# Kernel optimization log

Measured on AMD Instinct MI355X. Metric: run time of the kernel, lower is better.

The kernel has to match this reference:

```python
import jax, jax.numpy as jnp
import numpy as np

DIM = 768
NUM_HEADS = 12
HEAD_DIM = DIM // NUM_HEADS
SCALE = HEAD_DIM ** -0.5


def setup_inputs() -> dict:
    key = jax.random.key(0)
    k_x, k_qw, k_qb, k_pw, k_pb = jax.random.split(key, 5)
    B, S = 4, 2048
    x = jax.random.normal(k_x, (B, S, DIM), dtype=jnp.float32)
    # torch nn.Linear convention: weight shape [out_features, in_features]
    qkv_w = jax.random.normal(k_qw, (2 * DIM, DIM), dtype=jnp.float32) * 0.02
    qkv_b = jax.random.normal(k_qb, (2 * DIM,), dtype=jnp.float32) * 0.02
    proj_w = jax.random.normal(k_pw, (DIM, DIM), dtype=jnp.float32) * 0.02
    proj_b = jax.random.normal(k_pb, (DIM,), dtype=jnp.float32) * 0.02
    return {"x": x, "qkv_w": qkv_w, "qkv_b": qkv_b, "proj_w": proj_w, "proj_b": proj_b}


def reference(x, qkv_w, qkv_b, proj_w, proj_b):
    B, S, D = x.shape
    H, Hd = NUM_HEADS, HEAD_DIM
    # qkv projection -> (B, S, 2*D)
    qkv = jnp.einsum('bsd,ed->bse', x, qkv_w) + qkv_b
    # reshape to (B, S, 2, H, Hd) then split q, v with heads leading: (B, H, S, Hd)
    qkv = qkv.reshape(B, S, 2, H, Hd).transpose(2, 0, 3, 1, 4)
    q, v = qkv[0], qkv[1]
    q = q * SCALE
    # shared Q=K scores: (B, H, S, S)
    attn = jnp.einsum('bhid,bhjd->bhij', q, q)
    attn = jax.nn.softmax(attn, axis=-1)  # attn_drop p=0 (identity)
    out = jnp.einsum('bhij,bhjd->bhid', attn, v)
    out = out.transpose(0, 2, 1, 3).reshape(B, S, D)
    out = jnp.einsum('bsd,ed->bse', out, proj_w) + proj_b  # proj_drop p=0
    return out
```

## Files before the change

kernel.cpp:

```cpp
#include <hip/hip_runtime.h>
#include <hip/hip_bf16.h>

#define NH 12
#define HD 64
#define SEQ 2048
#define DM 768

typedef __attribute__((ext_vector_type(8))) short bf16x8;
typedef __attribute__((ext_vector_type(4))) short bf16x4;
typedef __attribute__((ext_vector_type(4))) float f32x4;

static __device__ __forceinline__ unsigned short f2bf(float f) {
  unsigned int u = __float_as_uint(f);
  u += 0x7fff + ((u >> 16) & 1);
  return (unsigned short)(u >> 16);
}

static __device__ __forceinline__ unsigned cvt_pk_bf16(float lo, float hi) {
  unsigned r;
  asm("v_cvt_pk_bf16_f32 %0, %1, %2" : "=v"(r) : "v"(lo), "v"(hi));
  return r;
}

static __device__ __forceinline__ void gload_lds16(const void* g, void* l) {
  __builtin_amdgcn_global_load_lds(
      (const __attribute__((address_space(1))) void*)g,
      (__attribute__((address_space(3))) void*)l, 16, 0, 0);
}

static __device__ __forceinline__ bf16x8 cat4(bf16x4 a, bf16x4 b) {
  bf16x8 r;
  r[0] = a[0]; r[1] = a[1]; r[2] = a[2]; r[3] = a[3];
  r[4] = b[0]; r[5] = b[1]; r[6] = b[2]; r[7] = b[3];
  return r;
}

#define QSCALE 0.15014030f

__global__ __launch_bounds__(256) void cvt3_kernel(
    const float* __restrict__ s0, unsigned short* __restrict__ d0, int n0,
    const float* __restrict__ s1, unsigned short* __restrict__ d1, int n1,
    const float* __restrict__ s2, unsigned short* __restrict__ d2, int n2) {
  int i = blockIdx.x * 256 + threadIdx.x;
  const int stride = gridDim.x * 256;
  const int ntot = n0 + n1 + n2;
  for (; i < ntot; i += stride) {
    const float* src;
    unsigned short* dst;
    int j = i;
    if (j < n0) { src = s0; dst = d0; }
    else if (j < n0 + n1) { j -= n0; src = s1; dst = d1; }
    else { j -= n0 + n1; src = s2; dst = d2; }
    const float4 a = reinterpret_cast<const float4*>(src)[j * 2];
    const float4 b = reinterpret_cast<const float4*>(src)[j * 2 + 1];
    ushort4 lo = make_ushort4(f2bf(a.x), f2bf(a.y), f2bf(a.z), f2bf(a.w));
    ushort4 hi = make_ushort4(f2bf(b.x), f2bf(b.y), f2bf(b.z), f2bf(b.w));
    reinterpret_cast<ushort4*>(dst)[j * 2] = lo;
    reinterpret_cast<ushort4*>(dst)[j * 2 + 1] = hi;
  }
}

__global__ __launch_bounds__(256) void qkv_kernel(
    const unsigned short* __restrict__ xb, const unsigned short* __restrict__ wb,
    const float* __restrict__ bias,
    unsigned short* __restrict__ qb, unsigned short* __restrict__ vtb) {
  __shared__ alignas(16) char As[2][8192];
  __shared__ alignas(16) char Bs[2][8192];
  const int tid = threadIdx.x;
  const int lane = tid & 63, wid = tid >> 6;
  const int wr = wid >> 1, wc = wid & 1;
  const int g = lane >> 4, c = lane & 15;
  const int m0 = blockIdx.x * 128, n0 = blockIdx.y * 128;
  const char* Ab = (const char*)xb;
  const char* Bb = (const char*)wb;

  const int o0 = tid * 16, o1 = tid * 16 + 4096;
  const int r0 = o0 >> 6, r1 = o1 >> 6;
  const int sw0 = (o0 & 63) ^ (((r0 >> 1) & 3) << 4);
  const int sw1 = (o1 & 63) ^ (((r1 >> 1) & 3) << 4);

  auto stage = [&](int kt, int buf) {
    const int k0b = kt * 64;
    gload_lds16(Ab + (size_t)(m0 + r0) * 1536 + k0b + sw0, &As[buf][o0]);
    gload_lds16(Bb + (size_t)(n0 + r0) * 1536 + k0b + sw0, &Bs[buf][o0]);
    gload_lds16(Ab + (size_t)(m0 + r1) * 1536 + k0b + sw1, &As[buf][o1]);
    gload_lds16(Bb + (size_t)(n0 + r1) * 1536 + k0b + sw1, &Bs[buf][o1]);
  };

  f32x4 acc[4][4] = {};
  stage(0, 0);

  for (int kt = 0; kt < 24; ++kt) {
    __syncthreads();
    if (kt < 23) stage(kt + 1, (kt + 1) & 1);
    const char* Ap = As[kt & 1];
    const char* Bp = Bs[kt & 1];
    bf16x8 a_f[4], b_f[4];
#pragma unroll
    for (int i = 0; i < 4; ++i) {
      const int ra = wr * 64 + i * 16 + c;
      const int rb = wc * 64 + i * 16 + c;
      a_f[i] = *reinterpret_cast<const bf16x8*>(Ap + ra * 64 + ((g ^ ((ra >> 1) & 3)) << 4));
      b_f[i] = *reinterpret_cast<const bf16x8*>(Bp + rb * 64 + ((g ^ ((rb >> 1) & 3)) << 4));
    }
#pragma unroll
    for (int ai = 0; ai < 4; ++ai)
#pragma unroll
      for (int ni = 0; ni < 4; ++ni)
        acc[ai][ni] = __builtin_amdgcn_mfma_f32_16x16x32_bf16(a_f[ai], b_f[ni], acc[ai][ni], 0, 0, 0);
  }

#pragma unroll
  for (int ni = 0; ni < 4; ++ni) {
    const int n = n0 + wc * 64 + ni * 16 + c;
    const float bn = bias[n];
    if (n < DM) {
      const int h = n >> 6, d = n & 63;
#pragma unroll
      for (int ai = 0; ai < 4; ++ai)
#pragma unroll
        for (int r = 0; r < 4; ++r) {
          const int m = m0 + wr * 64 + ai * 16 + g * 4 + r;
          const int bb = m >> 11, s = m & 2047;
          qb[(((size_t)(bb * NH + h)) * SEQ + s) * HD + d] = f2bf((acc[ai][ni][r] + bn) * QSCALE);
        }
    } else {
      const int nn = n - DM;
      const int h = nn >> 6, d = nn & 63;
#pragma unroll
      for (int ai = 0; ai < 4; ++ai) {
        const int m_base = m0 + wr * 64 + ai * 16 + g * 4;
        const int bb = m_base >> 11, s0 = m_base & 2047;
        const int blk = s0 >> 5, off = s0 & 31;
        const int offp = (((off >> 4) & 1) << 2) + (((off >> 2) & 3) << 3);
        ushort4 pk = make_ushort4(f2bf(acc[ai][ni][0] + bn), f2bf(acc[ai][ni][1] + bn),
                                  f2bf(acc[ai][ni][2] + bn), f2bf(acc[ai][ni][3] + bn));
        *reinterpret_cast<ushort4*>(
            &vtb[((size_t)(bb * NH + h) * HD + d) * SEQ + blk * 32 + offp]) = pk;
      }
    }
  }
}

__global__ __launch_bounds__(256, 4) void attn_kernel(
    const unsigned short* __restrict__ qb, const unsigned short* __restrict__ vtb,
    unsigned short* __restrict__ ao) {
  __shared__ alignas(16) char pool[2][16384];

  const int tid = threadIdx.x;
  const int lane = tid & 63, wid = tid >> 6;
  const int g = lane >> 4, c = lane & 15;
  const int wq = wid >> 1, wk = wid & 1;

  const int wg = blockIdx.x;
  const int xcd = wg & 7;
  const int idx = wg >> 3;
  const int bh = xcd * 6 + (idx >> 5);
  const int qs0 = (idx & 31) * 64;
  const size_t base = (size_t)bh * SEQ * HD;

  bf16x8 qf[2][2];
#pragma unroll
  for (int jq = 0; jq < 2; ++jq) {
    const unsigned short* qrow = &qb[base + (size_t)(qs0 + wq * 32 + jq * 16 + c) * HD + g * 8];
    qf[jq][0] = *reinterpret_cast<const bf16x8*>(qrow);
    qf[jq][1] = *reinterpret_cast<const bf16x8*>(qrow + 32);
  }

  const char* qbB = (const char*)qb;
  const char* vtB = (const char*)vtb;
  const int oK0 = tid * 16, oK1 = tid * 16 + 4096;
  const int swK0 = oK0 ^ (((oK0 >> 7) & 7) << 4);
  const int swK1 = oK1 ^ (((oK1 >> 7) & 7) << 4);
  const int rV0 = oK0 >> 7, rV1 = oK1 >> 7;
  const int swV0 = (oK0 & 127) ^ ((rV0 & 7) << 4);
  const int swV1 = (oK1 & 127) ^ ((rV1 & 7) << 4);

  auto stage = [&](int t, int buf) {
    char* P = pool[buf];
    const size_t kQ = base * 2 + (size_t)t * 8192;
    gload_lds16(qbB + kQ + swK0, P + oK0);
    gload_lds16(qbB + kQ + swK1, P + oK1);
    gload_lds16(vtB + ((size_t)(bh * HD + rV0) * SEQ + t * 64) * 2 + swV0, P + 8192 + oK0);
    gload_lds16(vtB + ((size_t)(bh * HD + rV1) * SEQ + t * 64) * 2 + swV1, P + 8192 + oK1);
  };

  float l_p[2] = {0.f, 0.f};
  f32x4 o_acc[4][2] = {};

  const int cswz = (c & 7) << 4;

  stage(0, 0);
  asm volatile("s_waitcnt vmcnt(0)" ::: "memory");
  __builtin_amdgcn_sched_barrier(0);
  __builtin_amdgcn_s_barrier();

  for (int t = 0; t < 32; ++t) {
    const char* P = pool[t & 1];
    if (t < 31) stage(t + 1, (t + 1) & 1);

    f32x4 sa[2][2] = {};
    __builtin_amdgcn_s_setprio(1);
#pragma unroll
    for (int jp = 0; jp < 2; ++jp) {
      const int krow = wk * 32 + jp * 16 + c;
      const bf16x8 kf0 = *reinterpret_cast<const bf16x8*>(P + krow * 128 + ((g * 16) ^ cswz));
      const bf16x8 kf1 = *reinterpret_cast<const bf16x8*>(P + krow * 128 + ((64 + g * 16) ^ cswz));
#pragma unroll
      for (int jq = 0; jq < 2; ++jq) {
        sa[jp][jq] = __builtin_amdgcn_mfma_f32_16x16x32_bf16(kf0, qf[jq][0], sa[jp][jq], 0, 0, 0);
        sa[jp][jq] = __builtin_amdgcn_mfma_f32_16x16x32_bf16(kf1, qf[jq][1], sa[jp][jq], 0, 0, 0);
      }
    }
    __builtin_amdgcn_s_setprio(0);

    bf16x4 pb[2][2];
#pragma unroll
    for (int jp = 0; jp < 2; ++jp)
#pragma unroll
      for (int jq = 0; jq < 2; ++jq) {
        float p0 = __builtin_amdgcn_exp2f(sa[jp][jq][0]);
        float p1 = __builtin_amdgcn_exp2f(sa[jp][jq][1]);
        float p2 = __builtin_amdgcn_exp2f(sa[jp][jq][2]);
        float p3 = __builtin_amdgcn_exp2f(sa[jp][jq][3]);
        l_p[jq] += (p0 + p1) + (p2 + p3);
        uint2 wv = make_uint2(cvt_pk_bf16(p0, p1), cvt_pk_bf16(p2, p3));
        pb[jp][jq] = *reinterpret_cast<bf16x4*>(&wv);
      }

    bf16x8 pvv[2];
    pvv[0] = cat4(pb[0][0], pb[1][0]);
    pvv[1] = cat4(pb[0][1], pb[1][1]);
    __builtin_amdgcn_s_setprio(1);
#pragma unroll
    for (int dn = 0; dn < 4; ++dn) {
      const int vrow = dn * 16 + c;
      const bf16x8 av = *reinterpret_cast<const bf16x8*>(
          P + 8192 + vrow * 128 + ((wk * 64 + 16 * g) ^ ((vrow & 7) << 4)));
#pragma unroll
      for (int jq = 0; jq < 2; ++jq)
        o_acc[dn][jq] = __builtin_amdgcn_mfma_f32_16x16x32_bf16(av, pvv[jq], o_acc[dn][jq], 0, 0, 0);
    }
    __builtin_amdgcn_s_setprio(0);

    asm volatile("s_waitcnt vmcnt(0)" ::: "memory");
    __builtin_amdgcn_sched_barrier(0);
    __builtin_amdgcn_s_barrier();
  }

#pragma unroll
  for (int jq = 0; jq < 2; ++jq) {
    float v = l_p[jq];
    v += __shfl_xor(v, 16);
    v += __shfl_xor(v, 32);
    l_p[jq] = v;
  }

  float* ex = (float*)(pool[0] + wq * 16384);
  float* exl = ex + 32 * 68;
  if (wk == 1) {
#pragma unroll
    for (int dn = 0; dn < 4; ++dn)
#pragma unroll
      for (int jq = 0; jq < 2; ++jq)
        *reinterpret_cast<f32x4*>(&ex[(jq * 16 + c) * 68 + dn * 16 + 4 * g]) = o_acc[dn][jq];
    if (g == 0) {
      exl[c] = l_p[0];
      exl[16 + c] = l_p[1];
    }
  }
  __syncthreads();
  if (wk == 0) {
    const int b = bh / NH, h = bh % NH;
    float linv[2];
#pragma unroll
    for (int jq = 0; jq < 2; ++jq)
      linv[jq] = __builtin_amdgcn_rcpf(l_p[jq] + exl[jq * 16 + c]);
#pragma unroll
    for (int dn = 0; dn < 4; ++dn)
#pragma unroll
      for (int jq = 0; jq < 2; ++jq) {
        f32x4 o = o_acc[dn][jq];
        o += *reinterpret_cast<const f32x4*>(&ex[(jq * 16 + c) * 68 + dn * 16 + 4 * g]);
        uint2 wv = make_uint2(cvt_pk_bf16(o[0] * linv[jq], o[1] * linv[jq]),
                              cvt_pk_bf16(o[2] * linv[jq], o[3] * linv[jq]));
        *reinterpret_cast<uint2*>(
            &ao[((size_t)b * SEQ + qs0 + wq * 32 + jq * 16 + c) * DM + h * HD + dn * 16 + 4 * g]) = wv;
      }
  }
}

__global__ __launch_bounds__(256) void proj_kernel(
    const unsigned short* __restrict__ ao, const unsigned short* __restrict__ pwb,
    const float* __restrict__ bias, float* __restrict__ out) {
  __shared__ alignas(16) char As[2][8192];
  __shared__ alignas(16) char Bs[2][8192];
  const int tid = threadIdx.x;
  const int lane = tid & 63, wid = tid >> 6;
  const int wr = wid >> 1, wc = wid & 1;
  const int g = lane >> 4, c = lane & 15;
  const int m0 = blockIdx.x * 128, n0 = blockIdx.y * 128;
  const char* Ab = (const char*)ao;
  const char* Bb = (const char*)pwb;

  const int o0 = tid * 16, o1 = tid * 16 + 4096;
  const int r0 = o0 >> 6, r1 = o1 >> 6;
  const int sw0 = (o0 & 63) ^ (((r0 >> 1) & 3) << 4);
  const int sw1 = (o1 & 63) ^ (((r1 >> 1) & 3) << 4);

  auto stage = [&](int kt, int buf) {
    const int k0b = kt * 64;
    gload_lds16(Ab + (size_t)(m0 + r0) * 1536 + k0b + sw0, &As[buf][o0]);
    gload_lds16(Bb + (size_t)(n0 + r0) * 1536 + k0b + sw0, &Bs[buf][o0]);
    gload_lds16(Ab + (size_t)(m0 + r1) * 1536 + k0b + sw1, &As[buf][o1]);
    gload_lds16(Bb + (size_t)(n0 + r1) * 1536 + k0b + sw1, &Bs[buf][o1]);
  };

  f32x4 acc[4][4] = {};
  stage(0, 0);

  for (int kt = 0; kt < 24; ++kt) {
    __syncthreads();
    if (kt < 23) stage(kt + 1, (kt + 1) & 1);
    const char* Ap = As[kt & 1];
    const char* Bp = Bs[kt & 1];
    bf16x8 a_f[4], b_f[4];
#pragma unroll
    for (int i = 0; i < 4; ++i) {
      const int ra = wr * 64 + i * 16 + c;
      const int rb = wc * 64 + i * 16 + c;
      a_f[i] = *reinterpret_cast<const bf16x8*>(Ap + ra * 64 + ((g ^ ((ra >> 1) & 3)) << 4));
      b_f[i] = *reinterpret_cast<const bf16x8*>(Bp + rb * 64 + ((g ^ ((rb >> 1) & 3)) << 4));
    }
#pragma unroll
    for (int ai = 0; ai < 4; ++ai)
#pragma unroll
      for (int ni = 0; ni < 4; ++ni)
        acc[ai][ni] = __builtin_amdgcn_mfma_f32_16x16x32_bf16(a_f[ai], b_f[ni], acc[ai][ni], 0, 0, 0);
  }

#pragma unroll
  for (int ni = 0; ni < 4; ++ni) {
    const int n = n0 + wc * 64 + ni * 16 + c;
    const float bn = bias[n];
#pragma unroll
    for (int ai = 0; ai < 4; ++ai)
#pragma unroll
      for (int r = 0; r < 4; ++r) {
        const int m = m0 + wr * 64 + ai * 16 + g * 4 + r;
        out[(size_t)m * DM + n] = acc[ai][ni][r] + bn;
      }
  }
}

extern "C" void kernel_launch(void* const* d_in, const int* in_sizes, int n_in,
                              void* d_out, int out_size, void* d_ws, size_t ws_size,
                              hipStream_t stream) {
  const float* x = (const float*)d_in[0];
  const float* qkv_w = (const float*)d_in[1];
  const float* qkv_b = (const float*)d_in[2];
  const float* proj_w = (const float*)d_in[3];
  const float* proj_b = (const float*)d_in[4];
  float* out = (float*)d_out;

  const size_t elems = (size_t)4 * NH * SEQ * HD;
  unsigned short* qbuf = (unsigned short*)d_ws;
  unsigned short* vtbuf = qbuf + elems;
  unsigned short* xbf = vtbuf + elems;
  unsigned short* aobuf = xbf;
  unsigned short* wqkvbf = xbf + elems;
  unsigned short* wprojbf = wqkvbf + (size_t)2 * DM * DM;

  cvt3_kernel<<<dim3(2048), 256, 0, stream>>>(
      x, xbf, (int)(elems / 8),
      qkv_w, wqkvbf, 2 * DM * DM / 8,
      proj_w, wprojbf, DM * DM / 8);

  qkv_kernel<<<dim3(64, 12), 256, 0, stream>>>(xbf, wqkvbf, qkv_b, qbuf, vtbuf);
  attn_kernel<<<dim3(1536), 256, 0, stream>>>(qbuf, vtbuf, aobuf);
  proj_kernel<<<dim3(64, 6), 256, 0, stream>>>(aobuf, wprojbf, proj_b, out);
}
```

Baseline: 124.2 us.

## Shrink proj tile to 64x128, raise attn occupancy, pack P directly

The projection GEMM now uses a 64x128 output tile per block, with each wave covering 64 rows by 32 columns, and launches twice as many blocks (768 instead of 384) to fill more CUs. The attention kernel's launch bounds are raised to 5 waves per SIMD, and the softmax probabilities are packed straight into 8-element bf16 vectors without the intermediate concatenation. The smaller proj tile improves parallelism but lowers operand reuse per block. The tighter register budget in attention could cause spills.

```diff
diff --git a/kernel.cpp b/kernel.cpp
--- a/kernel.cpp
+++ b/kernel.cpp
@@ -26,13 +26,6 @@
   __builtin_amdgcn_global_load_lds(
       (const __attribute__((address_space(1))) void*)g,
       (__attribute__((address_space(3))) void*)l, 16, 0, 0);
-}
-
-static __device__ __forceinline__ bf16x8 cat4(bf16x4 a, bf16x4 b) {
-  bf16x8 r;
-  r[0] = a[0]; r[1] = a[1]; r[2] = a[2]; r[3] = a[3];
-  r[4] = b[0]; r[5] = b[1]; r[6] = b[2]; r[7] = b[3];
-  return r;
 }
 
 #define QSCALE 0.15014030f
@@ -142,7 +135,7 @@
   }
 }
 
-__global__ __launch_bounds__(256, 4) void attn_kernel(
+__global__ __launch_bounds__(256, 5) void attn_kernel(
     const unsigned short* __restrict__ qb, const unsigned short* __restrict__ vtb,
     unsigned short* __restrict__ ao) {
   __shared__ alignas(16) char pool[2][16384];
@@ -214,23 +207,23 @@
     }
     __builtin_amdgcn_s_setprio(0);
 
-    bf16x4 pb[2][2];
-#pragma unroll
-    for (int jp = 0; jp < 2; ++jp)
-#pragma unroll
-      for (int jq = 0; jq < 2; ++jq) {
-        float p0 = __builtin_amdgcn_exp2f(sa[jp][jq][0]);
-        float p1 = __builtin_amdgcn_exp2f(sa[jp][jq][1]);
-        float p2 = __builtin_amdgcn_exp2f(sa[jp][jq][2]);
-        float p3 = __builtin_amdgcn_exp2f(sa[jp][jq][3]);
-        l_p[jq] += (p0 + p1) + (p2 + p3);
-        uint2 wv = make_uint2(cvt_pk_bf16(p0, p1), cvt_pk_bf16(p2, p3));
-        pb[jp][jq] = *reinterpret_cast<bf16x4*>(&wv);
-      }
-
     bf16x8 pvv[2];
-    pvv[0] = cat4(pb[0][0], pb[1][0]);
-    pvv[1] = cat4(pb[0][1], pb[1][1]);
+#pragma unroll
+    for (int jq = 0; jq < 2; ++jq) {
+      float a0 = __builtin_amdgcn_exp2f(sa[0][jq][0]);
+      float a1 = __builtin_amdgcn_exp2f(sa[0][jq][1]);
+      float a2 = __builtin_amdgcn_exp2f(sa[0][jq][2]);
+      float a3 = __builtin_amdgcn_exp2f(sa[0][jq][3]);
+      float b0 = __builtin_amdgcn_exp2f(sa[1][jq][0]);
+      float b1 = __builtin_amdgcn_exp2f(sa[1][jq][1]);
+      float b2 = __builtin_amdgcn_exp2f(sa[1][jq][2]);
+      float b3 = __builtin_amdgcn_exp2f(sa[1][jq][3]);
+      l_p[jq] += ((a0 + a1) + (a2 + a3)) + ((b0 + b1) + (b2 + b3));
+      uint4 u = make_uint4(cvt_pk_bf16(a0, a1), cvt_pk_bf16(a2, a3),
+                           cvt_pk_bf16(b0, b1), cvt_pk_bf16(b2, b3));
+      pvv[jq] = *reinterpret_cast<bf16x8*>(&u);
+    }
+
     __builtin_amdgcn_s_setprio(1);
 #pragma unroll
     for (int dn = 0; dn < 4; ++dn) {
@@ -293,30 +286,31 @@
 __global__ __launch_bounds__(256) void proj_kernel(
     const unsigned short* __restrict__ ao, const unsigned short* __restrict__ pwb,
     const float* __restrict__ bias, float* __restrict__ out) {
-  __shared__ alignas(16) char As[2][8192];
+  __shared__ alignas(16) char As[2][4096];
   __shared__ alignas(16) char Bs[2][8192];
   const int tid = threadIdx.x;
   const int lane = tid & 63, wid = tid >> 6;
-  const int wr = wid >> 1, wc = wid & 1;
   const int g = lane >> 4, c = lane & 15;
-  const int m0 = blockIdx.x * 128, n0 = blockIdx.y * 128;
+  const int m0 = blockIdx.x * 64, n0 = blockIdx.y * 128;
   const char* Ab = (const char*)ao;
   const char* Bb = (const char*)pwb;
 
-  const int o0 = tid * 16, o1 = tid * 16 + 4096;
-  const int r0 = o0 >> 6, r1 = o1 >> 6;
-  const int sw0 = (o0 & 63) ^ (((r0 >> 1) & 3) << 4);
-  const int sw1 = (o1 & 63) ^ (((r1 >> 1) & 3) << 4);
+  const int oA = tid * 16;
+  const int rA = oA >> 6;
+  const int swA = (oA & 63) ^ (((rA >> 1) & 3) << 4);
+  const int oB0 = tid * 16, oB1 = tid * 16 + 4096;
+  const int rB0 = oB0 >> 6, rB1 = oB1 >> 6;
+  const int swB0 = (oB0 & 63) ^ (((rB0 >> 1) & 3) << 4);
+  const int swB1 = (oB1 & 63) ^ (((rB1 >> 1) & 3) << 4);
 
   auto stage = [&](int kt, int buf) {
     const int k0b = kt * 64;
-    gload_lds16(Ab + (size_t)(m0 + r0) * 1536 + k0b + sw0, &As[buf][o0]);
-    gload_lds16(Bb + (size_t)(n0 + r0) * 1536 + k0b + sw0, &Bs[buf][o0]);
-    gload_lds16(Ab + (size_t)(m0 + r1) * 1536 + k0b + sw1, &As[buf][o1]);
-    gload_lds16(Bb + (size_t)(n0 + r1) * 1536 + k0b + sw1, &Bs[buf][o1]);
+    gload_lds16(Ab + (size_t)(m0 + rA) * 1536 + k0b + swA, &As[buf][oA]);
+    gload_lds16(Bb + (size_t)(n0 + rB0) * 1536 + k0b + swB0, &Bs[buf][oB0]);
+    gload_lds16(Bb + (size_t)(n0 + rB1) * 1536 + k0b + swB1, &Bs[buf][oB1]);
   };
 
-  f32x4 acc[4][4] = {};
+  f32x4 acc[4][2] = {};
   stage(0, 0);
 
   for (int kt = 0; kt < 24; ++kt) {
@@ -324,31 +318,34 @@
     if (kt < 23) stage(kt + 1, (kt + 1) & 1);
     const char* Ap = As[kt & 1];
     const char* Bp = Bs[kt & 1];
-    bf16x8 a_f[4], b_f[4];
+    bf16x8 a_f[4], b_f[2];
 #pragma unroll
     for (int i = 0; i < 4; ++i) {
-      const int ra = wr * 64 + i * 16 + c;
-      const int rb = wc * 64 + i * 16 + c;
+      const int ra = i * 16 + c;
       a_f[i] = *reinterpret_cast<const bf16x8*>(Ap + ra * 64 + ((g ^ ((ra >> 1) & 3)) << 4));
-      b_f[i] = *reinterpret_cast<const bf16x8*>(Bp + rb * 64 + ((g ^ ((rb >> 1) & 3)) << 4));
-    }
-#pragma unroll
-    for (int ai = 0; ai < 4; ++ai)
-#pragma unroll
-      for (int ni = 0; ni < 4; ++ni)
-        acc[ai][ni] = __builtin_amdgcn_mfma_f32_16x16x32_bf16(a_f[ai], b_f[ni], acc[ai][ni], 0, 0, 0);
-  }
-
-#pragma unroll
-  for (int ni = 0; ni < 4; ++ni) {
-    const int n = n0 + wc * 64 + ni * 16 + c;
+    }
+#pragma unroll
+    for (int j = 0; j < 2; ++j) {
+      const int rb = wid * 32 + j * 16 + c;
+      b_f[j] = *reinterpret_cast<const bf16x8*>(Bp + rb * 64 + ((g ^ ((rb >> 1) & 3)) << 4));
+    }
+#pragma unroll
+    for (int i = 0; i < 4; ++i)
+#pragma unroll
+      for (int j = 0; j < 2; ++j)
+        acc[i][j] = __builtin_amdgcn_mfma_f32_16x16x32_bf16(a_f[i], b_f[j], acc[i][j], 0, 0, 0);
+  }
+
+#pragma unroll
+  for (int j = 0; j < 2; ++j) {
+    const int n = n0 + wid * 32 + j * 16 + c;
     const float bn = bias[n];
 #pragma unroll
-    for (int ai = 0; ai < 4; ++ai)
+    for (int i = 0; i < 4; ++i)
 #pragma unroll
       for (int r = 0; r < 4; ++r) {
-        const int m = m0 + wr * 64 + ai * 16 + g * 4 + r;
-        out[(size_t)m * DM + n] = acc[ai][ni][r] + bn;
+        const int m = m0 + i * 16 + g * 4 + r;
+        out[(size_t)m * DM + n] = acc[i][j][r] + bn;
       }
   }
 }
@@ -378,5 +375,5 @@
 
   qkv_kernel<<<dim3(64, 12), 256, 0, stream>>>(xbf, wqkvbf, qkv_b, qbuf, vtbuf);
   attn_kernel<<<dim3(1536), 256, 0, stream>>>(qbuf, vtbuf, aobuf);
-  proj_kernel<<<dim3(64, 6), 256, 0, stream>>>(aobuf, wprojbf, proj_b, out);
-}
+  proj_kernel<<<dim3(128, 6), 256, 0, stream>>>(aobuf, wprojbf, proj_b, out);
+}
```

New measurement: 123.1 us. About the same (-0.9%).
